# Kernel tuning notes

Hardware: AMD Instinct MI355X
Metric: run time of the kernel (lower is better)

Reference implementation:

```python
import jax, jax.numpy as jnp
import numpy as np

N_HEAD = 16

def setup_inputs() -> dict:
    key = jax.random.key(0)
    k1, k2, k3 = jax.random.split(key, 3)
    B, T, E = 4, 2048, 1024
    x = jax.random.normal(k1, (B, T, E), dtype=jnp.float32)
    w_attn = jax.random.normal(k2, (4 * E, E), dtype=jnp.float32) * (1.0 / np.sqrt(E))
    b_attn = jax.random.normal(k3, (4 * E,), dtype=jnp.float32) * 0.02
    return {"x": x, "w_attn": w_attn, "b_attn": b_attn}

def reference(x, w_attn, b_attn):
    B, T, C = x.shape
    H = N_HEAD
    D = C // H  # head_dim
    qkv = x @ w_attn.T + b_attn                      # [B,T,4C]
    q, k, v = qkv[..., :C], qkv[..., C:2*C], qkv[..., 2*C:3*C]  # 4th chunk unused
    q = q.reshape(B, T, H, D).transpose(0, 2, 1, 3)  # [B,H,T,D]
    k = k.reshape(B, T, H, D).transpose(0, 2, 1, 3)
    v = v.reshape(B, T, H, D).transpose(0, 2, 1, 3)
    scale = 1.0 / np.sqrt(D)
    attn = jnp.einsum('bhqd,bhkd->bhqk', q, k) * scale  # [B,H,T,T]
    causal = jnp.tril(jnp.ones((T, T), dtype=bool))
    attn = jnp.where(causal[None, None], attn, -jnp.inf)
    attn = jax.nn.softmax(attn, axis=-1)
    y = jnp.einsum('bhqk,bhkd->bhqd', attn, v)       # [B,H,T,D]
    return y.transpose(0, 2, 1, 3).reshape(B, T, C)
```

## Files before the change

kernel.cpp:

```cpp
#include <hip/hip_runtime.h>
#include <math.h>


using short8 = __attribute__((ext_vector_type(8))) short;
using f32x4  = __attribute__((ext_vector_type(4))) float;

__device__ __forceinline__ ushort f2bf(float f) {
    union { float f; unsigned u; } x{f};
    unsigned r = x.u + 0x7fffu + ((x.u >> 16) & 1u);
    return (ushort)(r >> 16);
}
__device__ __forceinline__ unsigned pack_bf16_ru(float a, float b) {
    union { float f; unsigned u; } x{a}, y{b};
    return __builtin_amdgcn_perm(y.u + 0x8000u, x.u + 0x8000u, 0x07060302u);
}

__device__ __forceinline__ void gload_lds16(const void* g, void* l) {
    __builtin_amdgcn_global_load_lds(
        (const __attribute__((address_space(1))) void*)g,
        (__attribute__((address_space(3))) void*)l, 16, 0, 0);
}

__global__ void cvt_all(const float* __restrict__ x, const float* __restrict__ w,
                        ushort* __restrict__ xb, ushort* __restrict__ wb) {
    int i = blockIdx.x * blockDim.x + threadIdx.x;
    const float* src; ushort* dst; int j;
    if (i < 2097152) { src = x; dst = xb; j = i; }
    else             { src = w; dst = wb; j = i - 2097152; if (j >= 786432) return; }
    float4 v = ((const float4*)src)[j];
    ushort4 o;
    o.x = f2bf(v.x); o.y = f2bf(v.y); o.z = f2bf(v.z); o.w = f2bf(v.w);
    ((ushort4*)dst)[j] = o;
}

__global__ __launch_bounds__(512) void qkv_gemm(
    const ushort* __restrict__ A, const ushort* __restrict__ W,
    const float* __restrict__ bias,
    ushort* __restrict__ Qo, ushort* __restrict__ Ko, ushort* __restrict__ Vt)
{
    __shared__ ushort As[2][256 * 64];
    __shared__ ushort Ws[2][192 * 64];
    const int id = (int)blockIdx.x;
    const int xcd = id & 7, s = id >> 3;
    const int bm = xcd * 4 + (s & 3);
    const int bn = s >> 2;
    const int tid = threadIdx.x;
    const int wave = tid >> 6, lane = tid & 63;
    const int quad = lane >> 4, l16 = lane & 15, l7 = l16 & 7;
    const int wr = wave >> 2, wc = wave & 3;

    const ushort* Abase = A + (size_t)(bm * 256) * 1024;
    const ushort* Wbase = W + (size_t)(bn * 192) * 1024;

    f32x4 acc[8][3];
#pragma unroll
    for (int i = 0; i < 8; i++)
#pragma unroll
        for (int j = 0; j < 3; j++) acc[i][j] = (f32x4){0.f, 0.f, 0.f, 0.f};

#define STAGE_A(BB, H, KC)                                                          \
    {                                                                               \
        _Pragma("unroll")                                                           \
        for (int j = 0; j < 2; j++) {                                               \
            const int rb = (H) * 128 + j * 64 + wave * 8;                           \
            const int r  = rb + (lane >> 3);                                        \
            const int cc = (lane & 7) ^ ((lane >> 3) & 7);                          \
            gload_lds16(Abase + (size_t)r * 1024 + (KC) + cc * 8, &As[BB][rb * 64]); \
        }                                                                           \
    }
#define STAGE_W(BB, S3, KC)                                                         \
    {                                                                               \
        const int rb = (S3) * 64 + wave * 8;                                        \
        const int r  = rb + (lane >> 3);                                            \
        const int cc = (lane & 7) ^ ((lane >> 3) & 7);                              \
        gload_lds16(Wbase + (size_t)r * 1024 + (KC) + cc * 8, &Ws[BB][rb * 64]);    \
    }

#define PHASE(BB, MS, NS)                                                           \
    {                                                                               \
        short8 af[4][2], wf[2];                                                     \
        _Pragma("unroll")                                                           \
        for (int mf = 0; mf < 4; mf++)                                              \
            _Pragma("unroll")                                                       \
            for (int kk = 0; kk < 2; kk++)                                          \
                af[mf][kk] = *(const short8*)&As[BB][((MS) * 128 + wr * 64 + mf * 16 + l16) * 64 + (((kk * 4 + quad) ^ l7) * 8)]; \
        _Pragma("unroll")                                                           \
        for (int kk = 0; kk < 2; kk++)                                              \
            wf[kk] = *(const short8*)&Ws[BB][((NS) * 64 + wc * 16 + l16) * 64 + (((kk * 4 + quad) ^ l7) * 8)]; \
        __builtin_amdgcn_s_setprio(1);                                              \
        _Pragma("unroll")                                                           \
        for (int kk = 0; kk < 2; kk++)                                              \
            _Pragma("unroll")                                                       \
            for (int mf = 0; mf < 4; mf++)                                          \
                acc[(MS) * 4 + mf][NS] = __builtin_amdgcn_mfma_f32_16x16x32_bf16(   \
                    af[mf][kk], wf[kk], acc[(MS) * 4 + mf][NS], 0, 0, 0);           \
        __builtin_amdgcn_s_setprio(0);                                              \
    }

#define VM(N)  asm volatile("s_waitcnt vmcnt(" #N ")" ::: "memory")
#define BAR    asm volatile("s_barrier" ::: "memory")

    STAGE_A(0, 0, 0);
    STAGE_W(0, 0, 0);
    STAGE_W(0, 1, 0);
    STAGE_W(0, 2, 0);
    STAGE_A(0, 1, 0);

    int buf = 0;
    for (int t = 0; t < 15; ++t, buf ^= 1) {
        const int kn = (t + 1) * 64;
        STAGE_A(buf ^ 1, 0, kn); VM(6); BAR; PHASE(buf, 0, 0);
        STAGE_W(buf ^ 1, 0, kn); VM(6); BAR; PHASE(buf, 0, 1);
        STAGE_W(buf ^ 1, 1, kn); VM(6); BAR; PHASE(buf, 0, 2);
        STAGE_W(buf ^ 1, 2, kn); VM(5); BAR; PHASE(buf, 1, 0);
        STAGE_A(buf ^ 1, 1, kn);        BAR; PHASE(buf, 1, 1);
                                        BAR; PHASE(buf, 1, 2);
    }
    VM(4); BAR; PHASE(1, 0, 0);
    VM(3); BAR; PHASE(1, 0, 1);
    VM(2); BAR; PHASE(1, 0, 2);
    VM(0); BAR; PHASE(1, 1, 0);
                PHASE(1, 1, 1);
                PHASE(1, 1, 2);

#undef STAGE_A
#undef STAGE_W
#undef PHASE
#undef VM
#undef BAR

    const float SCALE_Q = 0.125f * 1.4426950408889634f;
#pragma unroll
    for (int ms = 0; ms < 2; ms++)
#pragma unroll
    for (int mf = 0; mf < 4; mf++) {
        const int m0 = bm * 256 + ms * 128 + wr * 64 + mf * 16 + quad * 4;
        const int b0 = m0 >> 11, t0 = m0 & 2047;
#pragma unroll
        for (int ns = 0; ns < 3; ns++) {
            const int n = bn * 192 + ns * 64 + wc * 16 + l16;
            const float bv = bias[n];
            const f32x4 a = acc[ms * 4 + mf][ns];
            if (n < 1024) {
                const int h = n >> 6, d = n & 63;
#pragma unroll
                for (int r = 0; r < 4; r++)
                    Qo[((size_t)(b0 * 16 + h) * 2048 + t0 + r) * 64 + d] = f2bf((a[r] + bv) * SCALE_Q);
            } else if (n < 2048) {
                const int c = n - 1024, h = c >> 6, d = c & 63;
#pragma unroll
                for (int r = 0; r < 4; r++)
                    Ko[((size_t)(b0 * 16 + h) * 2048 + t0 + r) * 64 + d] = f2bf(a[r] + bv);
            } else {
                const int c = n - 2048, h = c >> 6, d = c & 63;
                uint2 pk;
                pk.x = pack_bf16_ru(a[0] + bv, a[1] + bv);
                pk.y = pack_bf16_ru(a[2] + bv, a[3] + bv);
                *(uint2*)&Vt[((size_t)(b0 * 16 + h) * 64 + d) * 2048 + t0] = pk;
            }
        }
    }
}

__global__ __launch_bounds__(256) void attn_fwd(
    const ushort* __restrict__ Q, const ushort* __restrict__ K,
    const ushort* __restrict__ Vt, float* __restrict__ out)
{
    __shared__ ushort Ks[2][64 * 64];
    __shared__ ushort Vs[2][64 * 64];
    __shared__ ushort Ps[4][16 * 64];
    const int id = (int)blockIdx.x;
    const int bh = id & 63;
    const int s  = id >> 6;
    const int g = s >> 2, r4 = s & 3;
    const int qt = (g == 0) ? 15 - r4 : (g == 1) ? 8 + r4 : (g == 2) ? 7 - r4 : r4;
    const int b = bh >> 4, h = bh & 15;
    const int wave = threadIdx.x >> 6, lane = threadIdx.x & 63;
    const int quad = lane >> 4, l16 = lane & 15, l7 = l16 & 7;

    const ushort* Kbh = K  + (size_t)bh * 2048 * 64;
    const ushort* Vbh = Vt + (size_t)bh * 64 * 2048;
    ushort* Pw = Ps[wave];

    int qb[2];
    qb[0] = qt * 128 + wave * 16;
    qb[1] = qb[0] + 64;

    short8 qf[2][2];
#pragma unroll
    for (int qg = 0; qg < 2; qg++) {
        const ushort* Qp = Q + ((size_t)bh * 2048 + qb[qg] + l16) * 64;
        qf[qg][0] = *(const short8*)(Qp + quad * 8);
        qf[qg][1] = *(const short8*)(Qp + 32 + quad * 8);
    }

    f32x4 o[2][4];
#pragma unroll
    for (int qg = 0; qg < 2; qg++)
#pragma unroll
        for (int dg = 0; dg < 4; dg++) o[qg][dg] = (f32x4){0.f, 0.f, 0.f, 0.f};
    float lsum[2] = {0.f, 0.f};

    const int ntiles = 2 * qt + 2;

#define STAGE(k0_, bf_)                                                              \
    {                                                                                \
        _Pragma("unroll")                                                            \
        for (int j = 0; j < 2; j++) {                                                \
            const int rb = wave * 16 + j * 8;                                        \
            const int r  = rb + (lane >> 3);                                         \
            const int cc = (lane & 7) ^ (r & 7);                                     \
            gload_lds16(Kbh + (size_t)((k0_) + r) * 64 + cc * 8, &Ks[bf_][rb * 64]); \
            gload_lds16(Vbh + (size_t)r * 2048 + (k0_) + cc * 8, &Vs[bf_][rb * 64]); \
        }                                                                            \
    }

    STAGE(0, 0);
    int buf = 0, k0 = 0;
    for (int it = 0; it < ntiles; ++it, k0 += 64, buf ^= 1) {
        __syncthreads();
        if (it + 1 < ntiles) STAGE(k0 + 64, buf ^ 1);
        if (k0 > qb[1] + 15) continue;

        const bool act0 = k0 <= qb[0] + 15;

        short8 kf[4][2];
#pragma unroll
        for (int t = 0; t < 4; t++)
#pragma unroll
            for (int dh = 0; dh < 2; dh++)
                kf[t][dh] = *(const short8*)&Ks[buf][(t * 16 + l16) * 64 + (((dh * 4 + quad) ^ l7) * 8)];
        short8 vf[2][4];
#pragma unroll
        for (int kg = 0; kg < 2; kg++) {
            const int pc = ((kg * 4 + quad) ^ l7) * 8;
#pragma unroll
            for (int dg = 0; dg < 4; dg++)
                vf[kg][dg] = *(const short8*)&Vs[buf][(dg * 16 + l16) * 64 + pc];
        }

#pragma unroll
        for (int qg = 0; qg < 2; qg++) {
            if (qg == 0 && !act0) continue;
            f32x4 sc[4];
#pragma unroll
            for (int t = 0; t < 4; t++) {
                f32x4 z = (f32x4){0.f, 0.f, 0.f, 0.f};
                z = __builtin_amdgcn_mfma_f32_16x16x32_bf16(kf[t][0], qf[qg][0], z, 0, 0, 0);
                z = __builtin_amdgcn_mfma_f32_16x16x32_bf16(kf[t][1], qf[qg][1], z, 0, 0, 0);
                sc[t] = z;
            }
            const int q = qb[qg] + l16;
            float p[16], ps = 0.f;
            if (k0 + 63 > qb[qg]) {
#pragma unroll
                for (int t = 0; t < 4; t++)
#pragma unroll
                    for (int r = 0; r < 4; r++) {
                        const int key = k0 + t * 16 + quad * 4 + r;
                        const float sv = (key <= q) ? sc[t][r] : -INFINITY;
                        p[t * 4 + r] = __builtin_amdgcn_exp2f(sv);
                    }
            } else {
#pragma unroll
                for (int t = 0; t < 4; t++)
#pragma unroll
                    for (int r = 0; r < 4; r++)
                        p[t * 4 + r] = __builtin_amdgcn_exp2f(sc[t][r]);
            }
#pragma unroll
            for (int i = 0; i < 16; i++) ps += p[i];
            lsum[qg] += ps;
#pragma unroll
            for (int t = 0; t < 4; t++) {
                uint2 pk;
                pk.x = pack_bf16_ru(p[t * 4 + 0], p[t * 4 + 1]);
                pk.y = pack_bf16_ru(p[t * 4 + 2], p[t * 4 + 3]);
                const int pc = ((2 * t + (quad >> 1)) ^ l7) * 8 + (quad & 1) * 4;
                *(uint2*)(Pw + l16 * 64 + pc) = pk;
            }
#pragma unroll
            for (int kg = 0; kg < 2; kg++) {
                short8 pf = *(const short8*)(Pw + l16 * 64 + (((kg * 4 + quad) ^ l7) * 8));
#pragma unroll
                for (int dg = 0; dg < 4; dg++)
                    o[qg][dg] = __builtin_amdgcn_mfma_f32_16x16x32_bf16(vf[kg][dg], pf, o[qg][dg], 0, 0, 0);
            }
        }
    }
#undef STAGE

#pragma unroll
    for (int qg = 0; qg < 2; qg++) {
        float l = lsum[qg];
        l += __shfl_xor(l, 16);
        l += __shfl_xor(l, 32);
        const float rinv = 1.f / l;
        float* op = out + ((size_t)(b * 2048 + qb[qg] + l16)) * 1024 + h * 64;
#pragma unroll
        for (int dg = 0; dg < 4; dg++) {
            float4 v;
            v.x = o[qg][dg][0] * rinv; v.y = o[qg][dg][1] * rinv;
            v.z = o[qg][dg][2] * rinv; v.w = o[qg][dg][3] * rinv;
            *(float4*)(op + dg * 16 + quad * 4) = v;
        }
    }
}

extern "C" void kernel_launch(void* const* d_in, const int* in_sizes, int n_in,
                              void* d_out, int out_size, void* d_ws, size_t ws_size,
                              hipStream_t stream) {
    const float* x    = (const float*)d_in[0];
    const float* w    = (const float*)d_in[1];
    const float* bias = (const float*)d_in[2];

    ushort* xb  = (ushort*)d_ws;
    ushort* wb  = xb + 8388608;
    ushort* Qb  = wb + 3145728;
    ushort* Kb  = Qb + 8388608;
    ushort* Vtb = Kb + 8388608;

    cvt_all<<<11264, 256, 0, stream>>>(x, w, xb, wb);
    qkv_gemm<<<512, 512, 0, stream>>>(xb, wb, bias, Qb, Kb, Vtb);
    attn_fwd<<<1024, 256, 0, stream>>>(Qb, Kb, Vtb, (float*)d_out);
}
```

Measured before the change: 239.3 us.

## Enlarge QKV GEMM N-tile to 256 and restructure 8-phase LDS pipeline

Grows the QKV projection tile from 256x192 to 256x256, so each wave computes a 64x32 sub-tile with two B fragments per A fragment and the grid drops from 512 to 384 blocks. The main loop is rewritten as an 8-phase schedule over two K-steps that interleaves LDS reads, async global-to-LDS staging and MFMA blocks, using sched_barrier and builtin barriers. The aim is more MFMA work per LDS byte and fewer blocks. In exchange it uses more LDS and registers, and 384 blocks may fill the CUs less evenly than 512 did.

New measurement: 233.9 us. 1.02x faster.

```diff
diff --git a/kernel.cpp b/kernel.cpp
--- a/kernel.cpp
+++ b/kernel.cpp
@@ -39,7 +39,7 @@
     ushort* __restrict__ Qo, ushort* __restrict__ Ko, ushort* __restrict__ Vt)
 {
     __shared__ ushort As[2][256 * 64];
-    __shared__ ushort Ws[2][192 * 64];
+    __shared__ ushort Ws[2][256 * 64];
     const int id = (int)blockIdx.x;
     const int xcd = id & 7, s = id >> 3;
     const int bm = xcd * 4 + (s & 3);
@@ -50,13 +50,13 @@
     const int wr = wave >> 2, wc = wave & 3;
 
     const ushort* Abase = A + (size_t)(bm * 256) * 1024;
-    const ushort* Wbase = W + (size_t)(bn * 192) * 1024;
-
-    f32x4 acc[8][3];
+    const ushort* Wbase = W + (size_t)(bn * 256) * 1024;
+
+    f32x4 acc[8][4];
 #pragma unroll
     for (int i = 0; i < 8; i++)
 #pragma unroll
-        for (int j = 0; j < 3; j++) acc[i][j] = (f32x4){0.f, 0.f, 0.f, 0.f};
+        for (int j = 0; j < 4; j++) acc[i][j] = (f32x4){0.f, 0.f, 0.f, 0.f};
 
 #define STAGE_A(BB, H, KC)                                                          \
     {                                                                               \
@@ -68,66 +68,84 @@
             gload_lds16(Abase + (size_t)r * 1024 + (KC) + cc * 8, &As[BB][rb * 64]); \
         }                                                                           \
     }
-#define STAGE_W(BB, S3, KC)                                                         \
+#define STAGE_W(BB, H, KC)                                                          \
     {                                                                               \
-        const int rb = (S3) * 64 + wave * 8;                                        \
-        const int r  = rb + (lane >> 3);                                            \
-        const int cc = (lane & 7) ^ ((lane >> 3) & 7);                              \
-        gload_lds16(Wbase + (size_t)r * 1024 + (KC) + cc * 8, &Ws[BB][rb * 64]);    \
-    }
-
-#define PHASE(BB, MS, NS)                                                           \
+        _Pragma("unroll")                                                           \
+        for (int j = 0; j < 2; j++) {                                               \
+            const int rb = (H) * 128 + j * 64 + wave * 8;                           \
+            const int r  = rb + (lane >> 3);                                        \
+            const int cc = (lane & 7) ^ ((lane >> 3) & 7);                          \
+            gload_lds16(Wbase + (size_t)r * 1024 + (KC) + cc * 8, &Ws[BB][rb * 64]); \
+        }                                                                           \
+    }
+
+#define DSL(BB, MS, NS)                                                             \
     {                                                                               \
-        short8 af[4][2], wf[2];                                                     \
         _Pragma("unroll")                                                           \
         for (int mf = 0; mf < 4; mf++)                                              \
             _Pragma("unroll")                                                       \
             for (int kk = 0; kk < 2; kk++)                                          \
                 af[mf][kk] = *(const short8*)&As[BB][((MS) * 128 + wr * 64 + mf * 16 + l16) * 64 + (((kk * 4 + quad) ^ l7) * 8)]; \
         _Pragma("unroll")                                                           \
-        for (int kk = 0; kk < 2; kk++)                                              \
-            wf[kk] = *(const short8*)&Ws[BB][((NS) * 64 + wc * 16 + l16) * 64 + (((kk * 4 + quad) ^ l7) * 8)]; \
+        for (int nf = 0; nf < 2; nf++)                                              \
+            _Pragma("unroll")                                                       \
+            for (int kk = 0; kk < 2; kk++)                                          \
+                wf[nf][kk] = *(const short8*)&Ws[BB][((NS) * 128 + wc * 32 + nf * 16 + l16) * 64 + (((kk * 4 + quad) ^ l7) * 8)]; \
+    }
+
+#define MM(MS, NS)                                                                  \
+    {                                                                               \
         __builtin_amdgcn_s_setprio(1);                                              \
         _Pragma("unroll")                                                           \
         for (int kk = 0; kk < 2; kk++)                                              \
             _Pragma("unroll")                                                       \
             for (int mf = 0; mf < 4; mf++)                                          \
-                acc[(MS) * 4 + mf][NS] = __builtin_amdgcn_mfma_f32_16x16x32_bf16(   \
-                    af[mf][kk], wf[kk], acc[(MS) * 4 + mf][NS], 0, 0, 0);           \
+                _Pragma("unroll")                                                   \
+                for (int nf = 0; nf < 2; nf++)                                      \
+                    acc[(MS) * 4 + mf][(NS) * 2 + nf] = __builtin_amdgcn_mfma_f32_16x16x32_bf16( \
+                        af[mf][kk], wf[nf][kk], acc[(MS) * 4 + mf][(NS) * 2 + nf], 0, 0, 0); \
         __builtin_amdgcn_s_setprio(0);                                              \
     }
 
-#define VM(N)  asm volatile("s_waitcnt vmcnt(" #N ")" ::: "memory")
-#define BAR    asm volatile("s_barrier" ::: "memory")
-
-    STAGE_A(0, 0, 0);
-    STAGE_W(0, 0, 0);
-    STAGE_W(0, 1, 0);
-    STAGE_W(0, 2, 0);
-    STAGE_A(0, 1, 0);
-
-    int buf = 0;
-    for (int t = 0; t < 15; ++t, buf ^= 1) {
-        const int kn = (t + 1) * 64;
-        STAGE_A(buf ^ 1, 0, kn); VM(6); BAR; PHASE(buf, 0, 0);
-        STAGE_W(buf ^ 1, 0, kn); VM(6); BAR; PHASE(buf, 0, 1);
-        STAGE_W(buf ^ 1, 1, kn); VM(6); BAR; PHASE(buf, 0, 2);
-        STAGE_W(buf ^ 1, 2, kn); VM(5); BAR; PHASE(buf, 1, 0);
-        STAGE_A(buf ^ 1, 1, kn);        BAR; PHASE(buf, 1, 1);
-                                        BAR; PHASE(buf, 1, 2);
-    }
-    VM(4); BAR; PHASE(1, 0, 0);
-    VM(3); BAR; PHASE(1, 0, 1);
-    VM(2); BAR; PHASE(1, 0, 2);
-    VM(0); BAR; PHASE(1, 1, 0);
-                PHASE(1, 1, 1);
-                PHASE(1, 1, 2);
+#define VM(N)  asm volatile("s_waitcnt vmcnt(" #N ")")
+#define SCB    __builtin_amdgcn_sched_barrier(0)
+#define BARB   __builtin_amdgcn_s_barrier()
+
+    STAGE_W(0, 0, 0); STAGE_A(0, 0, 0); STAGE_A(0, 1, 0); STAGE_W(0, 1, 0);
+    STAGE_W(1, 0, 64); STAGE_A(1, 0, 64);
+    VM(4); SCB; BARB;
+
+    for (int i = 0; i < 7; ++i) {
+        const int kB = (2 * i + 1) * 64, kC = kB + 64, kD = kC + 64;
+        short8 af[4][2], wf[2][2];
+        DSL(0, 0, 0); STAGE_A(1, 1, kB); BARB; MM(0, 0); BARB;
+        DSL(0, 1, 0); STAGE_W(1, 1, kB); BARB; MM(1, 0); BARB;
+        DSL(0, 0, 1); STAGE_W(0, 0, kC); BARB; MM(0, 1); BARB;
+        DSL(0, 1, 1); STAGE_A(0, 0, kC); BARB; MM(1, 1); VM(4); SCB; BARB;
+        DSL(1, 0, 0); STAGE_A(0, 1, kC); BARB; MM(0, 0); BARB;
+        DSL(1, 1, 0); STAGE_W(0, 1, kC); BARB; MM(1, 0); BARB;
+        DSL(1, 0, 1); STAGE_W(1, 0, kD); BARB; MM(0, 1); BARB;
+        DSL(1, 1, 1); STAGE_A(1, 0, kD); BARB; MM(1, 1); VM(4); SCB; BARB;
+    }
+    {
+        short8 af[4][2], wf[2][2];
+        DSL(0, 0, 0); STAGE_A(1, 1, 960); BARB; MM(0, 0); BARB;
+        DSL(0, 1, 0); STAGE_W(1, 1, 960); BARB; MM(1, 0); BARB;
+        DSL(0, 0, 1);                     BARB; MM(0, 1); BARB;
+        DSL(0, 1, 1);                     BARB; MM(1, 1); VM(4); SCB; BARB;
+        DSL(1, 0, 0);                     BARB; MM(0, 0); VM(2); SCB; BARB;
+        DSL(1, 1, 0);                     BARB; MM(1, 0); VM(0); SCB; BARB;
+        DSL(1, 0, 1);                     BARB; MM(0, 1); BARB;
+        DSL(1, 1, 1);                     BARB; MM(1, 1);
+    }
 
 #undef STAGE_A
 #undef STAGE_W
-#undef PHASE
+#undef DSL
+#undef MM
 #undef VM
-#undef BAR
+#undef SCB
+#undef BARB
 
     const float SCALE_Q = 0.125f * 1.4426950408889634f;
 #pragma unroll
@@ -137,10 +155,12 @@
         const int m0 = bm * 256 + ms * 128 + wr * 64 + mf * 16 + quad * 4;
         const int b0 = m0 >> 11, t0 = m0 & 2047;
 #pragma unroll
-        for (int ns = 0; ns < 3; ns++) {
-            const int n = bn * 192 + ns * 64 + wc * 16 + l16;
+        for (int ns = 0; ns < 2; ns++)
+#pragma unroll
+        for (int nf = 0; nf < 2; nf++) {
+            const int n = bn * 256 + ns * 128 + wc * 32 + nf * 16 + l16;
             const float bv = bias[n];
-            const f32x4 a = acc[ms * 4 + mf][ns];
+            const f32x4 a = acc[ms * 4 + mf][ns * 2 + nf];
             if (n < 1024) {
                 const int h = n >> 6, d = n & 63;
 #pragma unroll
@@ -321,6 +341,6 @@
     ushort* Vtb = Kb + 8388608;
 
     cvt_all<<<11264, 256, 0, stream>>>(x, w, xb, wb);
-    qkv_gemm<<<512, 512, 0, stream>>>(xb, wb, bias, Qb, Kb, Vtb);
+    qkv_gemm<<<384, 512, 0, stream>>>(xb, wb, bias, Qb, Kb, Vtb);
     attn_fwd<<<1024, 256, 0, stream>>>(Qb, Kb, Vtb, (float*)d_out);
 }
```
